# Kernel tuning notes

Measured on AMD Instinct MI355X. Metric: run time of the kernel, lower is better.

## Reference

```python
import jax, jax.numpy as jnp
import numpy as np

N = 2048      # nodes: 8 sequences x 256 tokens
E = 524288    # edges: dense attention graph, 8 * 256^2
H = 8         # heads
DK = 64       # per-head dim


def setup_inputs() -> dict:
    key = jax.random.key(0)
    k1, k2, k3, k4, k5 = jax.random.split(key, 5)
    q = jax.random.normal(k1, (N, H, DK), dtype=jnp.float32)
    k = jax.random.normal(k2, (N, H, DK), dtype=jnp.float32)
    v = jax.random.normal(k3, (N, H, DK), dtype=jnp.float32)
    edge_src = jax.random.randint(k4, (E,), 0, N, dtype=jnp.int32)
    edge_dst = jax.random.randint(k5, (E,), 0, N, dtype=jnp.int32)
    return {"q": q, "k": k, "v": v, "edge_src": edge_src, "edge_dst": edge_dst}


def reference(q, k, v, edge_src, edge_dst):
    # src_dot_dst('k','q','score'): per-edge dot product over head dim -> [E, H]
    score = jnp.einsum('ehd,ehd->eh', k[edge_src], q[edge_dst])
    # scaled_exp('score', sqrt(d_k)): exp(clamp(score / sqrt(d_k), -10, 10))
    score = jnp.exp(jnp.clip(score / jnp.sqrt(jnp.float32(DK)), -10.0, 10.0))
    # send_and_recv: wv = sum_dst(v_src * score), z = sum_dst(score)
    wv = jax.ops.segment_sum(v[edge_src] * score[:, :, None], edge_dst, num_segments=N)  # [N, H, DK]
    z = jax.ops.segment_sum(score, edge_dst, num_segments=N)  # [N, H]
    # post_func normalization: attention output per node
    return wv / z[:, :, None]
```

## Files before the change

### kernel.cpp

```cpp
#include <hip/hip_runtime.h>

#define NNODES 2048
#define NHEAD 8
#define DKDIM 64

typedef unsigned int uint;
typedef unsigned short ushort;
typedef unsigned char uchar;
typedef __fp16 h2 __attribute__((ext_vector_type(2)));
typedef __fp16 h8 __attribute__((ext_vector_type(8)));
typedef float f4 __attribute__((ext_vector_type(4)));

#define KSCALE 0.18033688011112042f
#define CLAMP2 14.426950408889634f

__device__ __forceinline__ uint pk2(float a, float b) {
    union { h2 h; uint u; } x; x.h = __builtin_amdgcn_cvt_pkrtz(a, b); return x.u;
}

__global__ void prep1(const float* __restrict__ k, uint4* __restrict__ kc,
                      uint4* __restrict__ A4) {
    int i = blockIdx.x * 256 + threadIdx.x;
    int dim8 = i & 7, node = (i >> 3) & 2047, h = i >> 14;
    const float* src = k + (size_t)node * 512 + h * 64 + dim8 * 8;
    float4 f0 = *(const float4*)src;
    float4 f1 = *(const float4*)(src + 4);
    uint4 o;
    o.x = pk2(f0.x * KSCALE, f0.y * KSCALE);
    o.y = pk2(f0.z * KSCALE, f0.w * KSCALE);
    o.z = pk2(f1.x * KSCALE, f1.y * KSCALE);
    o.w = pk2(f1.z * KSCALE, f1.w * KSCALE);
    kc[(h * 2048 + node) * 8 + dim8] = o;
    uint4 zz = {0u, 0u, 0u, 0u};
    A4[i] = zz;
    A4[i + 131072] = zz;
}

__global__ void prep2(const float* __restrict__ v, ushort* __restrict__ vt,
                      const int* __restrict__ es, const int* __restrict__ ed,
                      uint* __restrict__ A32, int E) {
    __shared__ float tile[64][65];
    int b = blockIdx.x;
    int t = threadIdx.x;
    if (b < 256) {
        int h = b & 7, tn = b >> 3;
        int nl = t >> 2, dq = (t & 3) * 16;
        const float* src = v + ((size_t)(tn * 64 + nl)) * 512 + h * 64 + dq;
#pragma unroll
        for (int i = 0; i < 4; ++i) {
            float4 f = *(const float4*)(src + i * 4);
            tile[nl][dq + i * 4 + 0] = f.x;
            tile[nl][dq + i * 4 + 1] = f.y;
            tile[nl][dq + i * 4 + 2] = f.z;
            tile[nl][dq + i * 4 + 3] = f.w;
        }
        __syncthreads();
        int dim = t >> 2, nq = (t & 3) * 16;
        uint wv[8];
#pragma unroll
        for (int i = 0; i < 8; ++i)
            wv[i] = pk2(tile[nq + 2 * i][dim], tile[nq + 2 * i + 1][dim]);
        char* base = (char*)vt + ((size_t)(b & 7) * 64 + dim) * 4096 + (b >> 3) * 128;
        int nb0 = (t & 3) * 2;
        uint4 lo = { wv[0], wv[1], wv[2], wv[3] };
        uint4 hi = { wv[4], wv[5], wv[6], wv[7] };
        *(uint4*)(base + nb0 * 16) = lo;
        *(uint4*)(base + nb0 * 16 + 16) = hi;
    } else {
        int i = (b - 256) * 256 + t;
        if (i < E) {
            uint idx = (uint)ed[i] * 2048u + (uint)es[i];
            atomicAdd(&A32[idx >> 2], 1u << ((idx & 3) * 8));
        }
    }
}

__global__ void __launch_bounds__(512, 1) attn_kernel(
    const float* __restrict__ q, const ushort* __restrict__ kc, const ushort* __restrict__ vt,
    const uchar* __restrict__ A8, float* __restrict__ out) {
    __shared__ __align__(16) char LK[2][2][8192];
    __shared__ __align__(16) char LV[2][2][8192];
    __shared__ __align__(16) char LA[2][2][5120];

    int b = blockIdx.x;
    int h = b & 7;
    int dst0 = (b >> 3) * 64;
    int t = threadIdx.x;
    int w = t >> 6, half = w >> 2, wq = w & 3;
    int l = t & 63, c = l & 15, g = l >> 4;
    int ht = t & 255;

    const char* kH = (const char*)kc + (size_t)h * 262144;
    const char* vH = (const char*)vt + (size_t)h * 262144;

    h8 qf[2];
    {
        const float* qp = q + (size_t)(dst0 + wq * 16 + c) * 512 + h * 64 + g * 8;
#pragma unroll
        for (int ch = 0; ch < 2; ++ch) {
            float4 f0 = *(const float4*)(qp + ch * 32);
            float4 f1 = *(const float4*)(qp + ch * 32 + 4);
            union { uint u[4]; h8 v; } U;
            U.u[0] = pk2(f0.x, f0.y); U.u[1] = pk2(f0.z, f0.w);
            U.u[2] = pk2(f1.x, f1.y); U.u[3] = pk2(f1.z, f1.w);
            qf[ch] = U.v;
        }
    }

    f4 of[4];
#pragma unroll
    for (int i = 0; i < 4; ++i) of[i] = (f4){0.f, 0.f, 0.f, 0.f};
    float z = 0.f;

    int r0 = ht >> 3, b0 = ht & 7;
    int ar_ = ht >> 2, as_ = ht & 3;
    int ts0 = half * 16;
    uint4 kr[2], vr[2], ar;

#pragma unroll
    for (int j = 0; j < 2; ++j) {
        int row = r0 + j * 32;
        kr[j] = *(const uint4*)(kH + (size_t)(ts0 * 64 + row) * 128 + b0 * 16);
        vr[j] = *(const uint4*)(vH + (size_t)row * 4096 + ts0 * 128 + b0 * 16);
        *(uint4*)(LK[half][0] + row * 128 + (b0 ^ (row & 7)) * 16) = kr[j];
        *(uint4*)(LV[half][0] + row * 128 + (b0 ^ (row & 7)) * 16) = vr[j];
    }
    ar = *(const uint4*)(A8 + (size_t)(dst0 + ar_) * 2048 + ts0 * 64 + as_ * 16);
    *(uint4*)(LA[half][0] + ar_ * 80 + as_ * 16) = ar;
    __syncthreads();

    int sl = c + 32 * (g & 1);
    bool hi = (g >> 1) != 0;

    for (int it = 0; it < 16; ++it) {
        int cur = it & 1;
        int ts = ts0 + it;
        if (it < 15) {
#pragma unroll
            for (int j = 0; j < 2; ++j) {
                int row = r0 + j * 32;
                kr[j] = *(const uint4*)(kH + (size_t)((ts + 1) * 64 + row) * 128 + b0 * 16);
                vr[j] = *(const uint4*)(vH + (size_t)row * 4096 + (ts + 1) * 128 + b0 * 16);
            }
            ar = *(const uint4*)(A8 + (size_t)(dst0 + ar_) * 2048 + (ts + 1) * 64 + as_ * 16);
        }

        f4 sacc[4];
#pragma unroll
        for (int i = 0; i < 4; ++i) sacc[i] = (f4){0.f, 0.f, 0.f, 0.f};
        __builtin_amdgcn_s_setprio(1);
#pragma unroll
        for (int nt = 0; nt < 4; ++nt)
#pragma unroll
            for (int ch = 0; ch < 2; ++ch) {
                h8 kf = *(const h8*)(LK[half][cur] + (nt * 16 + c) * 128 +
                                     (((ch * 4 + g) ^ (c & 7)) * 16));
                sacc[nt] = __builtin_amdgcn_mfma_f32_16x16x32_f16(kf, qf[ch], sacc[nt], 0, 0, 0);
            }
        __builtin_amdgcn_s_setprio(0);

        uint pw[4][2];
#pragma unroll
        for (int nt = 0; nt < 4; ++nt) {
            uint aw = *(const uint*)(LA[half][cur] + (wq * 16 + c) * 80 + nt * 16 + 4 * g);
            float e[4];
#pragma unroll
            for (int r = 0; r < 4; ++r) {
                float sc = fminf(fmaxf(sacc[nt][r], -CLAMP2), CLAMP2);
                e[r] = exp2f(sc) * (float)((aw >> (8 * r)) & 255u);
                z += e[r];
            }
            pw[nt][0] = pk2(e[0], e[1]);
            pw[nt][1] = pk2(e[2], e[3]);
        }

        h8 sf[2];
#pragma unroll
        for (int ch = 0; ch < 2; ++ch) {
            uint a0 = __shfl(pw[2 * ch][0], sl),      b0_ = __shfl(pw[2 * ch + 1][0], sl);
            uint a1 = __shfl(pw[2 * ch][1], sl),      b1_ = __shfl(pw[2 * ch + 1][1], sl);
            uint a2 = __shfl(pw[2 * ch][0], sl + 16), b2_ = __shfl(pw[2 * ch + 1][0], sl + 16);
            uint a3 = __shfl(pw[2 * ch][1], sl + 16), b3_ = __shfl(pw[2 * ch + 1][1], sl + 16);
            union { uint u[4]; h8 v; } S;
            S.u[0] = hi ? b0_ : a0;
            S.u[1] = hi ? b1_ : a1;
            S.u[2] = hi ? b2_ : a2;
            S.u[3] = hi ? b3_ : a3;
            sf[ch] = S.v;
        }

        __builtin_amdgcn_s_setprio(1);
#pragma unroll
        for (int nt = 0; nt < 4; ++nt)
#pragma unroll
            for (int ch = 0; ch < 2; ++ch) {
                h8 vf = *(const h8*)(LV[half][cur] + (nt * 16 + c) * 128 +
                                     (((ch * 4 + g) ^ (c & 7)) * 16));
                of[nt] = __builtin_amdgcn_mfma_f32_16x16x32_f16(vf, sf[ch], of[nt], 0, 0, 0);
            }
        __builtin_amdgcn_s_setprio(0);

        if (it < 15) {
            int nb = cur ^ 1;
#pragma unroll
            for (int j = 0; j < 2; ++j) {
                int row = r0 + j * 32;
                *(uint4*)(LK[half][nb] + row * 128 + (b0 ^ (row & 7)) * 16) = kr[j];
                *(uint4*)(LV[half][nb] + row * 128 + (b0 ^ (row & 7)) * 16) = vr[j];
            }
            *(uint4*)(LA[half][nb] + ar_ * 80 + as_ * 16) = ar;
        }
        __syncthreads();
    }

    z += __shfl_xor(z, 16);
    z += __shfl_xor(z, 32);

    float* CL = (float*)&LK[0][0][0];
    float* CLz = (float*)&LV[0][0][0];
    if (half == 1) {
#pragma unroll
        for (int nt = 0; nt < 4; ++nt)
#pragma unroll
            for (int r = 0; r < 4; ++r)
                CL[(wq * 16 + c) * 65 + nt * 16 + 4 * g + r] = of[nt][r];
        if (l < 16) CLz[wq * 16 + c] = z;
    }
    __syncthreads();
    if (half == 0) {
        float zt = 1.0f / (z + CLz[wq * 16 + c]);
#pragma unroll
        for (int nt = 0; nt < 4; ++nt)
#pragma unroll
            for (int r = 0; r < 4; ++r) {
                int idx = (wq * 16 + c) * 65 + nt * 16 + 4 * g + r;
                CL[idx] = (of[nt][r] + CL[idx]) * zt;
            }
    }
    __syncthreads();
#pragma unroll
    for (int j = 0; j < 8; ++j) {
        int i2 = w * 8 + j;
        out[(size_t)(dst0 + i2) * 512 + h * 64 + l] = CL[i2 * 65 + l];
    }
}


extern "C" void kernel_launch(void* const* d_in, const int* in_sizes, int n_in,
                              void* d_out, int out_size, void* d_ws, size_t ws_size,
                              hipStream_t stream) {
    const float* q = (const float*)d_in[0];
    const float* k = (const float*)d_in[1];
    const float* v = (const float*)d_in[2];
    const int* esrc = (const int*)d_in[3];
    const int* edst = (const int*)d_in[4];
    float* out = (float*)d_out;
    const int E = in_sizes[3];

    uchar* A8 = (uchar*)d_ws;
    ushort* kc = (ushort*)(A8 + (size_t)NNODES * NNODES);
    ushort* vt = kc + (size_t)NHEAD * NNODES * DKDIM;

    prep1<<<512, 256, 0, stream>>>(k, (uint4*)kc, (uint4*)A8);
    prep2<<<2304, 256, 0, stream>>>(v, vt, esrc, edst, (uint*)A8, E);
    attn_kernel<<<256, 512, 0, stream>>>(q, kc, vt, A8, out);
}
```

Measured before the change: 64.66 us.

## Switch attention MFMAs to 32x32x16 tiles with split-source reduction

Replaces the 16x16x32 MFMA tiling with 32x32x16 MFMAs. Each wave now computes a 32-source by 32-destination score tile and a 32x64 output slab, with a cheaper lane-xor-32 shuffle in place of the multi-shuffle transpose of probabilities. The final reduction becomes a four-stage serialized accumulate in shared memory across the wave groups, followed by vectorized normalized stores. The larger tiles aim to cut LDS fragment reads and shuffle overhead per FLOP. In exchange they raise accumulator register pressure and add extra barriers in the epilogue.

```diff
diff --git a/kernel.cpp b/kernel.cpp
--- a/kernel.cpp
+++ b/kernel.cpp
@@ -9,7 +9,7 @@
 typedef unsigned char uchar;
 typedef __fp16 h2 __attribute__((ext_vector_type(2)));
 typedef __fp16 h8 __attribute__((ext_vector_type(8)));
-typedef float f4 __attribute__((ext_vector_type(4)));
+typedef float f16v __attribute__((ext_vector_type(16)));
 
 #define KSCALE 0.18033688011112042f
 #define CLAMP2 14.426950408889634f
@@ -86,30 +86,33 @@
     int h = b & 7;
     int dst0 = (b >> 3) * 64;
     int t = threadIdx.x;
-    int w = t >> 6, half = w >> 2, wq = w & 3;
-    int l = t & 63, c = l & 15, g = l >> 4;
+    int w = t >> 6, half = w >> 2;
+    int u = w & 3, sr = u >> 1, dc = u & 1;
+    int l = t & 63, lm = l & 31, hi = l >> 5;
     int ht = t & 255;
 
     const char* kH = (const char*)kc + (size_t)h * 262144;
     const char* vH = (const char*)vt + (size_t)h * 262144;
 
-    h8 qf[2];
+    h8 qf[4];
     {
-        const float* qp = q + (size_t)(dst0 + wq * 16 + c) * 512 + h * 64 + g * 8;
-#pragma unroll
-        for (int ch = 0; ch < 2; ++ch) {
-            float4 f0 = *(const float4*)(qp + ch * 32);
-            float4 f1 = *(const float4*)(qp + ch * 32 + 4);
-            union { uint u[4]; h8 v; } U;
-            U.u[0] = pk2(f0.x, f0.y); U.u[1] = pk2(f0.z, f0.w);
-            U.u[2] = pk2(f1.x, f1.y); U.u[3] = pk2(f1.z, f1.w);
-            qf[ch] = U.v;
-        }
-    }
-
-    f4 of[4];
-#pragma unroll
-    for (int i = 0; i < 4; ++i) of[i] = (f4){0.f, 0.f, 0.f, 0.f};
+        const float* qp = q + (size_t)(dst0 + dc * 32 + lm) * 512 + h * 64 + hi * 8;
+#pragma unroll
+        for (int j = 0; j < 4; ++j) {
+            float4 f0 = *(const float4*)(qp + j * 16);
+            float4 f1 = *(const float4*)(qp + j * 16 + 4);
+            union { uint u4[4]; h8 v; } U;
+            U.u4[0] = pk2(f0.x, f0.y); U.u4[1] = pk2(f0.z, f0.w);
+            U.u4[2] = pk2(f1.x, f1.y); U.u4[3] = pk2(f1.z, f1.w);
+            qf[j] = U.v;
+        }
+    }
+
+    f16v of[2];
+#pragma unroll
+    for (int dg = 0; dg < 2; ++dg)
+#pragma unroll
+        for (int i = 0; i < 16; ++i) of[dg][i] = 0.f;
     float z = 0.f;
 
     int r0 = ht >> 3, b0 = ht & 7;
@@ -129,9 +132,6 @@
     *(uint4*)(LA[half][0] + ar_ * 80 + as_ * 16) = ar;
     __syncthreads();
 
-    int sl = c + 32 * (g & 1);
-    bool hi = (g >> 1) != 0;
-
     for (int it = 0; it < 16; ++it) {
         int cur = it & 1;
         int ts = ts0 + it;
@@ -145,59 +145,57 @@
             ar = *(const uint4*)(A8 + (size_t)(dst0 + ar_) * 2048 + (ts + 1) * 64 + as_ * 16);
         }
 
-        f4 sacc[4];
-#pragma unroll
-        for (int i = 0; i < 4; ++i) sacc[i] = (f4){0.f, 0.f, 0.f, 0.f};
+        f16v sacc;
+#pragma unroll
+        for (int i = 0; i < 16; ++i) sacc[i] = 0.f;
         __builtin_amdgcn_s_setprio(1);
 #pragma unroll
-        for (int nt = 0; nt < 4; ++nt)
-#pragma unroll
-            for (int ch = 0; ch < 2; ++ch) {
-                h8 kf = *(const h8*)(LK[half][cur] + (nt * 16 + c) * 128 +
-                                     (((ch * 4 + g) ^ (c & 7)) * 16));
-                sacc[nt] = __builtin_amdgcn_mfma_f32_16x16x32_f16(kf, qf[ch], sacc[nt], 0, 0, 0);
-            }
+        for (int j = 0; j < 4; ++j) {
+            h8 kf = *(const h8*)(LK[half][cur] + (sr * 32 + lm) * 128 +
+                                 (((2 * j + hi) ^ (lm & 7)) * 16));
+            sacc = __builtin_amdgcn_mfma_f32_32x32x16_f16(kf, qf[j], sacc, 0, 0, 0);
+        }
         __builtin_amdgcn_s_setprio(0);
 
-        uint pw[4][2];
-#pragma unroll
-        for (int nt = 0; nt < 4; ++nt) {
-            uint aw = *(const uint*)(LA[half][cur] + (wq * 16 + c) * 80 + nt * 16 + 4 * g);
-            float e[4];
-#pragma unroll
-            for (int r = 0; r < 4; ++r) {
-                float sc = fminf(fmaxf(sacc[nt][r], -CLAMP2), CLAMP2);
-                e[r] = exp2f(sc) * (float)((aw >> (8 * r)) & 255u);
-                z += e[r];
-            }
-            pw[nt][0] = pk2(e[0], e[1]);
-            pw[nt][1] = pk2(e[2], e[3]);
-        }
-
-        h8 sf[2];
-#pragma unroll
-        for (int ch = 0; ch < 2; ++ch) {
-            uint a0 = __shfl(pw[2 * ch][0], sl),      b0_ = __shfl(pw[2 * ch + 1][0], sl);
-            uint a1 = __shfl(pw[2 * ch][1], sl),      b1_ = __shfl(pw[2 * ch + 1][1], sl);
-            uint a2 = __shfl(pw[2 * ch][0], sl + 16), b2_ = __shfl(pw[2 * ch + 1][0], sl + 16);
-            uint a3 = __shfl(pw[2 * ch][1], sl + 16), b3_ = __shfl(pw[2 * ch + 1][1], sl + 16);
-            union { uint u[4]; h8 v; } S;
-            S.u[0] = hi ? b0_ : a0;
-            S.u[1] = hi ? b1_ : a1;
-            S.u[2] = hi ? b2_ : a2;
-            S.u[3] = hi ? b3_ : a3;
-            sf[ch] = S.v;
+        uint W[4][2];
+        {
+            const char* Ac = LA[half][cur];
+#pragma unroll
+            for (int G = 0; G < 4; ++G) {
+                uint aw = *(const uint*)(Ac + (dc * 32 + lm) * 80 + sr * 32 + G * 8 + 4 * hi);
+                float ee[4];
+#pragma unroll
+                for (int j2 = 0; j2 < 4; ++j2) {
+                    float sc = fminf(fmaxf(sacc[4 * G + j2], -CLAMP2), CLAMP2);
+                    ee[j2] = exp2f(sc) * (float)((aw >> (8 * j2)) & 255u);
+                    z += ee[j2];
+                }
+                W[G][0] = pk2(ee[0], ee[1]);
+                W[G][1] = pk2(ee[2], ee[3]);
+            }
+        }
+        uint Wx[4][2];
+#pragma unroll
+        for (int G = 0; G < 4; ++G) {
+            Wx[G][0] = __shfl_xor(W[G][0], 32);
+            Wx[G][1] = __shfl_xor(W[G][1], 32);
         }
 
         __builtin_amdgcn_s_setprio(1);
 #pragma unroll
-        for (int nt = 0; nt < 4; ++nt)
-#pragma unroll
-            for (int ch = 0; ch < 2; ++ch) {
-                h8 vf = *(const h8*)(LV[half][cur] + (nt * 16 + c) * 128 +
-                                     (((ch * 4 + g) ^ (c & 7)) * 16));
-                of[nt] = __builtin_amdgcn_mfma_f32_16x16x32_f16(vf, sf[ch], of[nt], 0, 0, 0);
-            }
+        for (int ks = 0; ks < 2; ++ks) {
+            union { uint u4[4]; h8 v; } S;
+            S.u4[0] = hi ? Wx[2 * ks + 1][0] : W[2 * ks][0];
+            S.u4[1] = hi ? Wx[2 * ks + 1][1] : W[2 * ks][1];
+            S.u4[2] = hi ? W[2 * ks + 1][0] : Wx[2 * ks][0];
+            S.u4[3] = hi ? W[2 * ks + 1][1] : Wx[2 * ks][1];
+#pragma unroll
+            for (int dg = 0; dg < 2; ++dg) {
+                h8 vf = *(const h8*)(LV[half][cur] + (dg * 32 + lm) * 128 +
+                                     (((sr * 4 + ks * 2 + hi) ^ (lm & 7)) * 16));
+                of[dg] = __builtin_amdgcn_mfma_f32_32x32x16_f16(vf, S.v, of[dg], 0, 0, 0);
+            }
+        }
         __builtin_amdgcn_s_setprio(0);
 
         if (it < 15) {
@@ -213,35 +211,40 @@
         __syncthreads();
     }
 
-    z += __shfl_xor(z, 16);
     z += __shfl_xor(z, 32);
 
     float* CL = (float*)&LK[0][0][0];
     float* CLz = (float*)&LV[0][0][0];
-    if (half == 1) {
-#pragma unroll
-        for (int nt = 0; nt < 4; ++nt)
-#pragma unroll
-            for (int r = 0; r < 4; ++r)
-                CL[(wq * 16 + c) * 65 + nt * 16 + 4 * g + r] = of[nt][r];
-        if (l < 16) CLz[wq * 16 + c] = z;
-    }
-    __syncthreads();
-    if (half == 0) {
-        float zt = 1.0f / (z + CLz[wq * 16 + c]);
-#pragma unroll
-        for (int nt = 0; nt < 4; ++nt)
-#pragma unroll
-            for (int r = 0; r < 4; ++r) {
-                int idx = (wq * 16 + c) * 65 + nt * 16 + 4 * g + r;
-                CL[idx] = (of[nt][r] + CL[idx]) * zt;
-            }
-    }
-    __syncthreads();
-#pragma unroll
-    for (int j = 0; j < 8; ++j) {
-        int i2 = w * 8 + j;
-        out[(size_t)(dst0 + i2) * 512 + h * 64 + l] = CL[i2 * 65 + l];
+    int gid = half * 2 + sr;
+    for (int p = 0; p < 4; ++p) {
+        if (gid == p) {
+#pragma unroll
+            for (int dg = 0; dg < 2; ++dg)
+#pragma unroll
+                for (int reg = 0; reg < 16; ++reg) {
+                    int dim = dg * 32 + (reg & 3) + 8 * (reg >> 2) + 4 * hi;
+                    int idx = (dc * 32 + lm) * 68 + dim;
+                    if (p == 0) CL[idx] = of[dg][reg];
+                    else CL[idx] += of[dg][reg];
+                }
+            if (hi == 0) {
+                if (p == 0) CLz[dc * 32 + lm] = z;
+                else CLz[dc * 32 + lm] += z;
+            }
+        }
+        __syncthreads();
+    }
+
+    {
+        int dst = t >> 3, d8 = t & 7;
+        float inv = 1.0f / CLz[dst];
+        float4 o0 = *(float4*)(CL + dst * 68 + d8 * 8);
+        float4 o1 = *(float4*)(CL + dst * 68 + d8 * 8 + 4);
+        o0.x *= inv; o0.y *= inv; o0.z *= inv; o0.w *= inv;
+        o1.x *= inv; o1.y *= inv; o1.z *= inv; o1.w *= inv;
+        float* op = out + (size_t)(dst0 + dst) * 512 + h * 64 + d8 * 8;
+        *(float4*)op = o0;
+        *(float4*)(op + 4) = o1;
     }
 }
 
```

After: 63.58 us. No clear change (-1.7%).
